# Optimization experiments

Hardware: AMD Instinct MI355X
Metric: run time of the kernel (lower is better)

## Reference

```python
import jax, jax.numpy as jnp
import numpy as np

B, NUMS, SEQ, H, LAYERS, PRED = 128, 128, 256, 1024, 2, 96


def setup_inputs() -> dict:
    key = jax.random.key(0)
    ks = jax.random.split(key, 7)
    s = 0.02
    return {
        "x": jax.random.normal(ks[0], (B, NUMS, SEQ), jnp.float32),
        "W0": jax.random.normal(ks[1], (NUMS + H, 4 * H), jnp.float32) * s,
        "b0": jax.random.normal(ks[2], (4 * H,), jnp.float32) * s,
        "W1": jax.random.normal(ks[3], (H + H, 4 * H), jnp.float32) * s,
        "b1": jax.random.normal(ks[4], (4 * H,), jnp.float32) * s,
        "fc_w": jax.random.normal(ks[5], (H, PRED), jnp.float32) * s,
        "fc_b": jax.random.normal(ks[6], (PRED,), jnp.float32) * s,
    }


def _lstm_layer(x_seq, W, b, h0, c0):
    # x_seq: [B, T, D]; W packs the four gate linears [D+H, 4H] (i,f,o,g)
    def step(carry, xt):
        h, c = carry
        z = jnp.concatenate([xt, h], axis=1) @ W + b  # [B, 4H]
        i, f, o, g = jnp.split(z, 4, axis=1)
        i, f, o = jax.nn.sigmoid(i), jax.nn.sigmoid(f), jax.nn.sigmoid(o)
        c = f * c + i * jnp.tanh(g)
        h = o * jnp.tanh(c)
        return (h, c), h

    (h, c), hs = jax.lax.scan(step, (h0, c0), jnp.swapaxes(x_seq, 0, 1))
    return jnp.swapaxes(hs, 0, 1), h, c  # [B, T, H], [B, H], [B, H]


def reference(x, W0, b0, W1, b1, fc_w, fc_b):
    bsz = x.shape[0]
    h = jnp.zeros((bsz, H), x.dtype)
    c = jnp.zeros((bsz, H), x.dtype)
    seq = jnp.swapaxes(x, 1, 2)  # [B, T, NUMS]
    # NB: faithful to source, (h, c) carry over across layers (no reset)
    seq, h, c = _lstm_layer(seq, W0, b0, h, c)
    seq, h, c = _lstm_layer(seq, W1, b1, h, c)
    out = jnp.tanh(seq[:, -1, :] @ fc_w + fc_b)  # [B, PRED]
    return (out, h, c)
```

## Files before the change

kernel.cpp:

```cpp
#include <hip/hip_runtime.h>
#include <stdint.h>

#define Bsz  128
#define NUMS 128
#define SEQn 256
#define Hn   1024
#define PRED 96
#define G4H  4096
#define GN   256
#define BH   ((size_t)Bsz*Hn)

typedef __attribute__((ext_vector_type(8))) short bf16x8;
typedef __attribute__((ext_vector_type(4))) float f32x4;

template<int N> struct IC { static constexpr int value = N; };

__device__ __forceinline__ unsigned short f2bf(float x){
  union { float f; unsigned u; } v; v.f = x;
  return (unsigned short)((v.u + 0x7FFFu + ((v.u >> 16) & 1u)) >> 16);
}
__device__ __forceinline__ float bf2f(unsigned short s){
  union { unsigned u; float f; } v; v.u = ((unsigned)s) << 16; return v.f;
}

__global__ void pack_x_kernel(const float* __restrict__ x, unsigned short* __restrict__ xp){
  __shared__ float tile[64][65];
  const int t0 = blockIdx.x * 64, n0 = blockIdx.y * 64, b = blockIdx.z;
  const int tid = threadIdx.x;
  const int c = tid & 63, r = tid >> 6;
  #pragma unroll
  for (int i = 0; i < 16; i++){
    int n = r + i*4;
    tile[n][c] = x[((size_t)b*NUMS + n0 + n)*SEQn + t0 + c];
  }
  __syncthreads();
  #pragma unroll
  for (int i = 0; i < 16; i++){
    int t = r + i*4;
    xp[((size_t)(t0+t)*Bsz + b)*NUMS + n0 + c] = f2bf(tile[c][t]);
  }
}

__global__ void pack_w_kernel(const float* __restrict__ W, unsigned short* __restrict__ Wpk,
                              int KST, int row_off, int kstride, int kof){
  const int u = blockIdx.x * blockDim.x + threadIdx.x;
  if (u >= 256*KST*64) return;
  const int lane = u & 63;
  const int kst  = (u >> 6) % KST;
  const int cgg  = (u >> 6) / KST;
  const int nb = cgg >> 2, gate = cgg & 3;
  const int col = gate*Hn + nb*16 + (lane & 15);
  const int kbase = row_off + kst*32 + (lane >> 4)*8;
  unsigned short tmp[8];
  #pragma unroll
  for (int e = 0; e < 8; e++) tmp[e] = f2bf(W[(size_t)(kbase+e)*G4H + col]);
  ((ulonglong2*)Wpk)[(size_t)(cgg*kstride + kof + kst)*64 + lane] = *(const ulonglong2*)tmp;
}

__global__ void zero_kernel(unsigned short* __restrict__ h0, float* __restrict__ c,
                            unsigned* __restrict__ bars){
  int i = blockIdx.x*256 + threadIdx.x;
  if (i < Bsz*Hn){ h0[i] = 0; c[i] = 0.0f; }
  if (i < 512) bars[i] = 0u;
}

template<int K1, int S2, int KTOT, int LAYER, bool RING2>
__global__ __launch_bounds__(512, 2)
void persist_kernel(const unsigned short* __restrict__ xpp,
                    unsigned short* __restrict__ hring,
                    unsigned short* __restrict__ h1b,
                    const unsigned short* __restrict__ Wpk,
                    const float* __restrict__ bias,
                    float* __restrict__ cst,
                    float* __restrict__ hf_out,
                    unsigned* __restrict__ bar)
{
  constexpr int KST_TOT = KTOT/32;
  constexpr int HALF = KST_TOT/2;
  constexpr int NCH = (KTOT + 511)/512;
  __shared__ union SM {
    struct { unsigned short a[2][32*512]; unsigned short xb[32*128]; } s;
    float e[2][4*32*18];
  } sm;
  const int tid = threadIdx.x;
  const int w = tid >> 6, l = tid & 63;
  const int blk = blockIdx.x;
  const int q = blk >> 3;
  const int nb = (blk & 7)*8 + (q & 7);
  const int mb = q >> 3;
  const int ksh = w & 1, cgi = w >> 1;
  const int cgg = nb*4 + cgi;
  const int lrow = l & 15, lg = l >> 4;

  bf16x8 wreg[HALF];
  #pragma unroll
  for (int j = 0; j < HALF; j++)
    wreg[j] = *(const bf16x8*)(Wpk + ((size_t)(cgg*KST_TOT + 2*j + ksh)*64 + l)*8);

  const int erow = tid >> 4, ejj = tid & 15;
  const int R = mb*32 + erow;
  const int J = nb*16 + ejj;
  const size_t idx = (size_t)R*Hn + J;
  float creg = (LAYER == 0) ? 0.f : cst[idx];

  for (int t = 0; t < SEQn; ++t){
    #pragma unroll
    for (int j = 0; j < HALF; j++) asm volatile("" : "+v"(wreg[j]));

    const unsigned short* A1;
    const unsigned short* A2;
    unsigned short* hout;
    if (LAYER == 0){
      A1   = hring + (size_t)t*BH;
      A2   = xpp + (size_t)t*Bsz*NUMS;
      hout = hring + (size_t)(t+1)*BH;
    } else {
      A1   = hring + (size_t)(t+1)*BH;
      A2   = (t == 0) ? (hring + (size_t)SEQn*BH)
                      : (h1b + (size_t)(RING2 ? (t-1) : ((t-1)&1))*BH);
      hout = h1b + (size_t)(RING2 ? t : (t&1))*BH;
    }

    f32x4 acc2[2] = {{0.f,0.f,0.f,0.f},{0.f,0.f,0.f,0.f}};

    auto stage = [&](int ch, int kw, int lu,
                     const unsigned short* A1p, const unsigned short* A2p){
      unsigned short* dst = (LAYER == 0 && ch == NCH-1) ? sm.s.xb : sm.s.a[ch & 1];
      const int nissue = kw >> 4;
      for (int i = w; i < nissue; i += 8){
        const int s = i*64 + l;
        const int row = s >> lu;
        const int uu  = s & ((1 << lu) - 1);
        const int ku  = uu ^ (row & 7);
        const int kg  = ch*512 + ku*8;
        const int Rr  = mb*32 + row;
        if (kg < K1){
          const unsigned short* src = A1p + (size_t)Rr*K1 + kg;
          __builtin_amdgcn_global_load_lds(
            (const __attribute__((address_space(1))) void*)src,
            (__attribute__((address_space(3))) void*)&dst[i*512], 16, 0, 0);
        } else {
          const unsigned short* src = A2p + (size_t)Rr*S2 + (kg - K1);
          if constexpr (LAYER == 1 && !RING2){
            __builtin_amdgcn_global_load_lds(
              (const __attribute__((address_space(1))) void*)src,
              (__attribute__((address_space(3))) void*)&dst[i*512], 16, 0, 17);
          } else {
            __builtin_amdgcn_global_load_lds(
              (const __attribute__((address_space(1))) void*)src,
              (__attribute__((address_space(3))) void*)&dst[i*512], 16, 0, 0);
          }
        }
      }
    };

    const bool pre01 = (LAYER == 1) && (t > 0);
    const bool preX  = (LAYER == 0) && (t > 0);
    if (!pre01){
      constexpr int kw0 = (KTOT >= 512) ? 512 : KTOT;
      stage(0, kw0, (kw0 == 512) ? 6 : 4, A1, A2);
    }
    __syncthreads();

    auto do_chunk = [&](auto CHC){
      constexpr int ch = decltype(CHC)::value;
      if constexpr (ch < NCH){
        constexpr int kw = ((KTOT - ch*512) >= 512) ? 512 : (KTOT - ch*512);
        if constexpr (ch + 1 < NCH){
          constexpr int kwn = ((KTOT - (ch+1)*512) >= 512) ? 512 : (KTOT - (ch+1)*512);
          const bool skip = (pre01 && (ch+1) == 1) || (preX && (ch+1) == NCH-1);
          if (!skip) stage(ch+1, kwn, (kwn == 512) ? 6 : 4, A1, A2);
        }
        constexpr int UPR  = kw >> 3;
        constexpr int nksl = kw >> 6;
        const unsigned short* abase = (LAYER == 0 && ch == NCH-1) ? sm.s.xb
                                                                  : sm.s.a[ch & 1];
        #pragma unroll
        for (int ksl = 0; ksl < nksl; ksl++){
          const int klocal = ksl*2 + ksh;
          const int unit = klocal*4 + lg;
          bf16x8 af0 = *(const bf16x8*)&abase[((lrow     )*UPR + (unit ^ (lrow & 7)))*8];
          bf16x8 af1 = *(const bf16x8*)&abase[((lrow + 16)*UPR + (unit ^ (lrow & 7)))*8];
          acc2[0] = __builtin_amdgcn_mfma_f32_16x16x32_bf16(af0, wreg[ch*8 + ksl], acc2[0], 0, 0, 0);
          acc2[1] = __builtin_amdgcn_mfma_f32_16x16x32_bf16(af1, wreg[ch*8 + ksl], acc2[1], 0, 0, 0);
        }
        __syncthreads();
      }
    };
    do_chunk(IC<0>{}); do_chunk(IC<1>{}); do_chunk(IC<2>{}); do_chunk(IC<3>{});

    {
      #pragma unroll
      for (int mi = 0; mi < 2; mi++)
        #pragma unroll
        for (int r = 0; r < 4; r++){
          const int row2 = mi*16 + lg*4 + r;
          sm.e[ksh][(cgi*32 + row2)*18 + lrow] = acc2[mi][r];
        }
    }
    __syncthreads();
    {
      float zi = sm.e[0][(0*32+erow)*18 + ejj] + sm.e[1][(0*32+erow)*18 + ejj];
      float zf = sm.e[0][(1*32+erow)*18 + ejj] + sm.e[1][(1*32+erow)*18 + ejj];
      float zo = sm.e[0][(2*32+erow)*18 + ejj] + sm.e[1][(2*32+erow)*18 + ejj];
      float zg = sm.e[0][(3*32+erow)*18 + ejj] + sm.e[1][(3*32+erow)*18 + ejj];
      zi += bias[0*Hn + J]; zf += bias[1*Hn + J];
      zo += bias[2*Hn + J]; zg += bias[3*Hn + J];
      const float gi = 1.f/(1.f + __expf(-zi));
      const float gf = 1.f/(1.f + __expf(-zf));
      const float go = 1.f/(1.f + __expf(-zo));
      const float gg = tanhf(zg);
      creg = gf * creg + gi * gg;
      const float hn = go * tanhf(creg);
      const unsigned hu   = (unsigned)f2bf(hn);
      const unsigned mate = (unsigned)__shfl_xor((int)hu, 1);
      if ((l & 1) == 0){
        const unsigned pk = hu | (mate << 16);
        __hip_atomic_store((unsigned*)(hout + idx), pk,
                           __ATOMIC_RELAXED, __HIP_MEMORY_SCOPE_AGENT);
      }
      if (t == SEQn-1){
        cst[idx] = creg;
        if (LAYER == 1) hf_out[idx] = hn;
      }
    }

    if (t + 1 < SEQn){
      __syncthreads();
      if (tid == 0)
        __hip_atomic_fetch_add(&bar[t], 1u, __ATOMIC_RELAXED, __HIP_MEMORY_SCOPE_AGENT);
      if constexpr (LAYER == 1){
        const unsigned short* A1n = hring + (size_t)(t+2)*BH;
        stage(0, 512, 6, A1n, A1n);
        stage(1, 512, 6, A1n, A1n);
      } else {
        stage(NCH-1, 128, 4, A1, xpp + (size_t)(t+1)*Bsz*NUMS);
      }
      if (tid == 0){
        while (__hip_atomic_load(&bar[t], __ATOMIC_RELAXED, __HIP_MEMORY_SCOPE_AGENT) < GN)
          __builtin_amdgcn_s_sleep(1);
      }
      __syncthreads();
    }
  }
}

__global__ __launch_bounds__(256)
void fc_out_kernel(const float* __restrict__ hf, const float* __restrict__ cst,
                   const float* __restrict__ fcw, const float* __restrict__ fcb,
                   float* __restrict__ dout){
  __shared__ float hrow[Hn];
  const int b = blockIdx.x, tid = threadIdx.x;
  for (int i = tid; i < Hn; i += 256) hrow[i] = hf[(size_t)b*Hn + i];
  __syncthreads();
  if (tid < PRED){
    float a = fcb[tid];
    for (int k = 0; k < Hn; k++) a += hrow[k] * fcw[(size_t)k*PRED + tid];
    dout[(size_t)b*PRED + tid] = tanhf(a);
  }
  for (int i = tid; i < Hn; i += 256){
    dout[Bsz*PRED + (size_t)b*Hn + i] = hf[(size_t)b*Hn + i];
    dout[Bsz*PRED + (size_t)Bsz*Hn + (size_t)b*Hn + i] = cst[(size_t)b*Hn + i];
  }
}

extern "C" void kernel_launch(void* const* d_in, const int* in_sizes, int n_in,
                              void* d_out, int out_size, void* d_ws, size_t ws_size,
                              hipStream_t stream){
  const float* x   = (const float*)d_in[0];
  const float* W0  = (const float*)d_in[1];
  const float* b0  = (const float*)d_in[2];
  const float* W1  = (const float*)d_in[3];
  const float* b1  = (const float*)d_in[4];
  const float* fcw = (const float*)d_in[5];
  const float* fcb = (const float*)d_in[6];
  float* dout = (float*)d_out;

  char* p = (char*)d_ws;
  auto alloc = [&](size_t bytes)->void*{
    void* r = (void*)p; p += (bytes + 255) & ~(size_t)255; return r;
  };
  unsigned short* xp   = (unsigned short*)alloc((size_t)SEQn*Bsz*NUMS*2);
  unsigned short* Wpk0 = (unsigned short*)alloc((size_t)256*36*64*8*2);
  unsigned short* Wpk1 = (unsigned short*)alloc((size_t)256*64*64*8*2);
  unsigned short* H0   = (unsigned short*)alloc((size_t)(SEQn+1)*BH*2);
  float* cst = (float*)alloc((size_t)BH*4);
  float* hf  = (float*)alloc((size_t)BH*4);
  unsigned* bars = (unsigned*)alloc((size_t)512*sizeof(unsigned));

  const bool big = ws_size >= (size_t)176*1024*1024;
  unsigned short* h1b;
  if (big) h1b = (unsigned short*)alloc((size_t)SEQn*BH*2);
  else     h1b = (unsigned short*)alloc((size_t)2*BH*2);

  pack_x_kernel<<<dim3(SEQn/64, NUMS/64, Bsz), dim3(256), 0, stream>>>(x, xp);
  pack_w_kernel<<<dim3((256*32*64 + 255)/256), dim3(256), 0, stream>>>(W0, Wpk0, 32, 128, 36, 0);
  pack_w_kernel<<<dim3((256*4*64  + 255)/256), dim3(256), 0, stream>>>(W0, Wpk0,  4,   0, 36, 32);
  pack_w_kernel<<<dim3((256*64*64 + 255)/256), dim3(256), 0, stream>>>(W1, Wpk1, 64, 0, 64, 0);
  zero_kernel<<<dim3((Bsz*Hn + 255)/256), dim3(256), 0, stream>>>(H0, cst, bars);

  persist_kernel<1024, NUMS, 1152, 0, false><<<dim3(GN), dim3(512), 0, stream>>>(
      xp, H0, nullptr, Wpk0, b0, cst, nullptr, bars);

  if (big){
    persist_kernel<1024, Hn, 2048, 1, true><<<dim3(GN), dim3(512), 0, stream>>>(
        nullptr, H0, h1b, Wpk1, b1, cst, hf, bars + 256);
  } else {
    persist_kernel<1024, Hn, 2048, 1, false><<<dim3(GN), dim3(512), 0, stream>>>(
        nullptr, H0, h1b, Wpk1, b1, cst, hf, bars + 256);
  }

  fc_out_kernel<<<dim3(Bsz), dim3(256), 0, stream>>>(hf, cst, fcw, fcb, dout);
}
```

Measured before the change: 3.528 ms.

## Split grid barrier per batch-row group and issue all chunk loads upfront with vmcnt waits

The global per-timestep barrier over all 256 blocks becomes four independent barriers, one per batch-row group (mb), since each group only depends on its own rows of h. Shared memory now holds every K chunk at once, so all async global-to-LDS loads are issued at the start of the step and consumed in order using explicit vmcnt waits, replacing the double-buffered chunk loop with its per-chunk __syncthreads. Bias loads are hoisted out of the time loop. The larger LDS footprint may hurt occupancy, and the hand-set vmcnt counts must match the issued load count exactly.

```diff
diff --git a/kernel.cpp b/kernel.cpp
--- a/kernel.cpp
+++ b/kernel.cpp
@@ -19,9 +19,11 @@
   union { float f; unsigned u; } v; v.f = x;
   return (unsigned short)((v.u + 0x7FFFu + ((v.u >> 16) & 1u)) >> 16);
 }
-__device__ __forceinline__ float bf2f(unsigned short s){
-  union { unsigned u; float f; } v; v.u = ((unsigned)s) << 16; return v.f;
-}
+
+#define WAITV(N) do { \
+  asm volatile("s_waitcnt vmcnt(" #N ")" ::: "memory"); \
+  __builtin_amdgcn_sched_barrier(0); \
+  __builtin_amdgcn_s_barrier(); } while(0)
 
 __global__ void pack_x_kernel(const float* __restrict__ x, unsigned short* __restrict__ xp){
   __shared__ float tile[64][65];
@@ -61,7 +63,7 @@
                             unsigned* __restrict__ bars){
   int i = blockIdx.x*256 + threadIdx.x;
   if (i < Bsz*Hn){ h0[i] = 0; c[i] = 0.0f; }
-  if (i < 512) bars[i] = 0u;
+  if (i < 2048) bars[i] = 0u;
 }
 
 template<int K1, int S2, int KTOT, int LAYER, bool RING2>
@@ -77,11 +79,11 @@
 {
   constexpr int KST_TOT = KTOT/32;
   constexpr int HALF = KST_TOT/2;
-  constexpr int NCH = (KTOT + 511)/512;
-  __shared__ union SM {
-    struct { unsigned short a[2][32*512]; unsigned short xb[32*128]; } s;
-    float e[2][4*32*18];
-  } sm;
+  constexpr int NFULL = (LAYER == 0) ? 2 : 4;
+  __shared__ unsigned short sa[NFULL][32*512];
+  __shared__ unsigned short sxb[(LAYER == 0) ? 32*128 : 64];
+  __shared__ float se[2][4*32*18];
+
   const int tid = threadIdx.x;
   const int w = tid >> 6, l = tid & 63;
   const int blk = blockIdx.x;
@@ -102,6 +104,48 @@
   const int J = nb*16 + ejj;
   const size_t idx = (size_t)R*Hn + J;
   float creg = (LAYER == 0) ? 0.f : cst[idx];
+  const float bI = bias[0*Hn + J], bF = bias[1*Hn + J];
+  const float bO = bias[2*Hn + J], bG = bias[3*Hn + J];
+
+  auto stageFull = [&](int ch, const unsigned short* A1p, const unsigned short* A2p){
+    unsigned short* dst = sa[ch];
+    #pragma unroll
+    for (int ii = 0; ii < 4; ii++){
+      const int i = ii*8 + w;
+      const int s = i*64 + l;
+      const int row = s >> 6, uu = s & 63;
+      const int ku  = uu ^ (row & 7);
+      const int kg  = ch*512 + ku*8;
+      const int Rr  = mb*32 + row;
+      if (kg < K1){
+        const unsigned short* src = A1p + (size_t)Rr*K1 + kg;
+        __builtin_amdgcn_global_load_lds(
+          (const __attribute__((address_space(1))) void*)src,
+          (__attribute__((address_space(3))) void*)&dst[i*512], 16, 0, 0);
+      } else {
+        const unsigned short* src = A2p + (size_t)Rr*S2 + (kg - K1);
+        if constexpr (LAYER == 1 && !RING2){
+          __builtin_amdgcn_global_load_lds(
+            (const __attribute__((address_space(1))) void*)src,
+            (__attribute__((address_space(3))) void*)&dst[i*512], 16, 0, 17);
+        } else {
+          __builtin_amdgcn_global_load_lds(
+            (const __attribute__((address_space(1))) void*)src,
+            (__attribute__((address_space(3))) void*)&dst[i*512], 16, 0, 0);
+        }
+      }
+    }
+  };
+  auto stageXB = [&](const unsigned short* A2p){
+    const int i = w;
+    const int s = i*64 + l;
+    const int row = s >> 4, uu = s & 15;
+    const int ku  = uu ^ (row & 7);
+    const unsigned short* src = A2p + (size_t)(mb*32 + row)*S2 + ku*8;
+    __builtin_amdgcn_global_load_lds(
+      (const __attribute__((address_space(1))) void*)src,
+      (__attribute__((address_space(3))) void*)&sxb[i*512], 16, 0, 0);
+  };
 
   for (int t = 0; t < SEQn; ++t){
     #pragma unroll
@@ -123,71 +167,46 @@
 
     f32x4 acc2[2] = {{0.f,0.f,0.f,0.f},{0.f,0.f,0.f,0.f}};
 
-    auto stage = [&](int ch, int kw, int lu,
-                     const unsigned short* A1p, const unsigned short* A2p){
-      unsigned short* dst = (LAYER == 0 && ch == NCH-1) ? sm.s.xb : sm.s.a[ch & 1];
-      const int nissue = kw >> 4;
-      for (int i = w; i < nissue; i += 8){
-        const int s = i*64 + l;
-        const int row = s >> lu;
-        const int uu  = s & ((1 << lu) - 1);
-        const int ku  = uu ^ (row & 7);
-        const int kg  = ch*512 + ku*8;
-        const int Rr  = mb*32 + row;
-        if (kg < K1){
-          const unsigned short* src = A1p + (size_t)Rr*K1 + kg;
-          __builtin_amdgcn_global_load_lds(
-            (const __attribute__((address_space(1))) void*)src,
-            (__attribute__((address_space(3))) void*)&dst[i*512], 16, 0, 0);
-        } else {
-          const unsigned short* src = A2p + (size_t)Rr*S2 + (kg - K1);
-          if constexpr (LAYER == 1 && !RING2){
-            __builtin_amdgcn_global_load_lds(
-              (const __attribute__((address_space(1))) void*)src,
-              (__attribute__((address_space(3))) void*)&dst[i*512], 16, 0, 17);
-          } else {
-            __builtin_amdgcn_global_load_lds(
-              (const __attribute__((address_space(1))) void*)src,
-              (__attribute__((address_space(3))) void*)&dst[i*512], 16, 0, 0);
-          }
-        }
+    if constexpr (LAYER == 1){
+      if (t == 0){ stageFull(0, A1, A2); stageFull(1, A1, A2); }
+      stageFull(2, A1, A2); stageFull(3, A1, A2);
+    } else {
+      if (t == 0) stageXB(A2);
+      stageFull(0, A1, A2); stageFull(1, A1, A2);
+    }
+
+    auto comp = [&](auto CHC){
+      constexpr int ch = decltype(CHC)::value;
+      const unsigned short* abase = sa[ch];
+      #pragma unroll
+      for (int ksl = 0; ksl < 8; ksl++){
+        const int klocal = ksl*2 + ksh;
+        const int unit = klocal*4 + lg;
+        bf16x8 af0 = *(const bf16x8*)&abase[((lrow     )*64 + (unit ^ (lrow & 7)))*8];
+        bf16x8 af1 = *(const bf16x8*)&abase[((lrow + 16)*64 + (unit ^ (lrow & 7)))*8];
+        acc2[0] = __builtin_amdgcn_mfma_f32_16x16x32_bf16(af0, wreg[ch*8 + ksl], acc2[0], 0, 0, 0);
+        acc2[1] = __builtin_amdgcn_mfma_f32_16x16x32_bf16(af1, wreg[ch*8 + ksl], acc2[1], 0, 0, 0);
       }
     };
 
-    const bool pre01 = (LAYER == 1) && (t > 0);
-    const bool preX  = (LAYER == 0) && (t > 0);
-    if (!pre01){
-      constexpr int kw0 = (KTOT >= 512) ? 512 : KTOT;
-      stage(0, kw0, (kw0 == 512) ? 6 : 4, A1, A2);
-    }
-    __syncthreads();
-
-    auto do_chunk = [&](auto CHC){
-      constexpr int ch = decltype(CHC)::value;
-      if constexpr (ch < NCH){
-        constexpr int kw = ((KTOT - ch*512) >= 512) ? 512 : (KTOT - ch*512);
-        if constexpr (ch + 1 < NCH){
-          constexpr int kwn = ((KTOT - (ch+1)*512) >= 512) ? 512 : (KTOT - (ch+1)*512);
-          const bool skip = (pre01 && (ch+1) == 1) || (preX && (ch+1) == NCH-1);
-          if (!skip) stage(ch+1, kwn, (kwn == 512) ? 6 : 4, A1, A2);
-        }
-        constexpr int UPR  = kw >> 3;
-        constexpr int nksl = kw >> 6;
-        const unsigned short* abase = (LAYER == 0 && ch == NCH-1) ? sm.s.xb
-                                                                  : sm.s.a[ch & 1];
-        #pragma unroll
-        for (int ksl = 0; ksl < nksl; ksl++){
-          const int klocal = ksl*2 + ksh;
-          const int unit = klocal*4 + lg;
-          bf16x8 af0 = *(const bf16x8*)&abase[((lrow     )*UPR + (unit ^ (lrow & 7)))*8];
-          bf16x8 af1 = *(const bf16x8*)&abase[((lrow + 16)*UPR + (unit ^ (lrow & 7)))*8];
-          acc2[0] = __builtin_amdgcn_mfma_f32_16x16x32_bf16(af0, wreg[ch*8 + ksl], acc2[0], 0, 0, 0);
-          acc2[1] = __builtin_amdgcn_mfma_f32_16x16x32_bf16(af1, wreg[ch*8 + ksl], acc2[1], 0, 0, 0);
-        }
-        __syncthreads();
-      }
-    };
-    do_chunk(IC<0>{}); do_chunk(IC<1>{}); do_chunk(IC<2>{}); do_chunk(IC<3>{});
+    if constexpr (LAYER == 1){
+      WAITV(12); comp(IC<0>{});
+      WAITV(8);  comp(IC<1>{});
+      WAITV(4);  comp(IC<2>{});
+      WAITV(0);  comp(IC<3>{});
+    } else {
+      WAITV(4);  comp(IC<0>{});
+      WAITV(0);  comp(IC<1>{});
+      #pragma unroll
+      for (int ksl = 0; ksl < 2; ksl++){
+        const int klocal = ksl*2 + ksh;
+        const int unit = klocal*4 + lg;
+        bf16x8 af0 = *(const bf16x8*)&sxb[((lrow     )*16 + (unit ^ (lrow & 7)))*8];
+        bf16x8 af1 = *(const bf16x8*)&sxb[((lrow + 16)*16 + (unit ^ (lrow & 7)))*8];
+        acc2[0] = __builtin_amdgcn_mfma_f32_16x16x32_bf16(af0, wreg[16 + ksl], acc2[0], 0, 0, 0);
+        acc2[1] = __builtin_amdgcn_mfma_f32_16x16x32_bf16(af1, wreg[16 + ksl], acc2[1], 0, 0, 0);
+      }
+    }
 
     {
       #pragma unroll
@@ -195,17 +214,15 @@
         #pragma unroll
         for (int r = 0; r < 4; r++){
           const int row2 = mi*16 + lg*4 + r;
-          sm.e[ksh][(cgi*32 + row2)*18 + lrow] = acc2[mi][r];
+          se[ksh][(cgi*32 + row2)*18 + lrow] = acc2[mi][r];
         }
     }
     __syncthreads();
     {
-      float zi = sm.e[0][(0*32+erow)*18 + ejj] + sm.e[1][(0*32+erow)*18 + ejj];
-      float zf = sm.e[0][(1*32+erow)*18 + ejj] + sm.e[1][(1*32+erow)*18 + ejj];
-      float zo = sm.e[0][(2*32+erow)*18 + ejj] + sm.e[1][(2*32+erow)*18 + ejj];
-      float zg = sm.e[0][(3*32+erow)*18 + ejj] + sm.e[1][(3*32+erow)*18 + ejj];
-      zi += bias[0*Hn + J]; zf += bias[1*Hn + J];
-      zo += bias[2*Hn + J]; zg += bias[3*Hn + J];
+      float zi = se[0][(0*32+erow)*18 + ejj] + se[1][(0*32+erow)*18 + ejj] + bI;
+      float zf = se[0][(1*32+erow)*18 + ejj] + se[1][(1*32+erow)*18 + ejj] + bF;
+      float zo = se[0][(2*32+erow)*18 + ejj] + se[1][(2*32+erow)*18 + ejj] + bO;
+      float zg = se[0][(3*32+erow)*18 + ejj] + se[1][(3*32+erow)*18 + ejj] + bG;
       const float gi = 1.f/(1.f + __expf(-zi));
       const float gf = 1.f/(1.f + __expf(-zf));
       const float go = 1.f/(1.f + __expf(-zo));
@@ -228,19 +245,21 @@
     if (t + 1 < SEQn){
       __syncthreads();
       if (tid == 0)
-        __hip_atomic_fetch_add(&bar[t], 1u, __ATOMIC_RELAXED, __HIP_MEMORY_SCOPE_AGENT);
+        __hip_atomic_fetch_add(&bar[t*4 + mb], 1u,
+                               __ATOMIC_RELAXED, __HIP_MEMORY_SCOPE_AGENT);
       if constexpr (LAYER == 1){
         const unsigned short* A1n = hring + (size_t)(t+2)*BH;
-        stage(0, 512, 6, A1n, A1n);
-        stage(1, 512, 6, A1n, A1n);
+        stageFull(0, A1n, A1n);
+        stageFull(1, A1n, A1n);
       } else {
-        stage(NCH-1, 128, 4, A1, xpp + (size_t)(t+1)*Bsz*NUMS);
+        stageXB(xpp + (size_t)(t+1)*Bsz*NUMS);
       }
       if (tid == 0){
-        while (__hip_atomic_load(&bar[t], __ATOMIC_RELAXED, __HIP_MEMORY_SCOPE_AGENT) < GN)
+        while (__hip_atomic_load(&bar[t*4 + mb], __ATOMIC_RELAXED,
+                                 __HIP_MEMORY_SCOPE_AGENT) < 64u)
           __builtin_amdgcn_s_sleep(1);
       }
-      __syncthreads();
+      __builtin_amdgcn_s_barrier();
     }
   }
 }
@@ -286,7 +305,7 @@
   unsigned short* H0   = (unsigned short*)alloc((size_t)(SEQn+1)*BH*2);
   float* cst = (float*)alloc((size_t)BH*4);
   float* hf  = (float*)alloc((size_t)BH*4);
-  unsigned* bars = (unsigned*)alloc((size_t)512*sizeof(unsigned));
+  unsigned* bars = (unsigned*)alloc((size_t)2048*sizeof(unsigned));
 
   const bool big = ws_size >= (size_t)176*1024*1024;
   unsigned short* h1b;
@@ -304,10 +323,10 @@
 
   if (big){
     persist_kernel<1024, Hn, 2048, 1, true><<<dim3(GN), dim3(512), 0, stream>>>(
-        nullptr, H0, h1b, Wpk1, b1, cst, hf, bars + 256);
+        nullptr, H0, h1b, Wpk1, b1, cst, hf, bars + 1024);
   } else {
     persist_kernel<1024, Hn, 2048, 1, false><<<dim3(GN), dim3(512), 0, stream>>>(
-        nullptr, H0, h1b, Wpk1, b1, cst, hf, bars + 256);
+        nullptr, H0, h1b, Wpk1, b1, cst, hf, bars + 1024);
   }
 
   fc_out_kernel<<<dim3(Bsz), dim3(256), 0, stream>>>(hf, cst, fcw, fcb, dout);
```

New measurement: 4.657 ms. 32.0% more time.

## Stage all K chunks in separate LDS buffers and drop per-chunk barriers

Applied to the files above, without the earlier changes.

Each K chunk now gets its own shared-memory buffer instead of ping-ponging two buffers. All chunks are issued up front, which removes the per-chunk __syncthreads. On later timesteps, work that depends on already-available data (the x input in layer 0, the layer-0 h in layer 1) is computed first while the recurrent-h chunks are loaded, leaving a single barrier before the remaining MFMAs. Layer 1 quadruples its A staging buffers, which raises LDS use and may limit the two-blocks-per-CU occupancy, and the barrier array is enlarged.

```diff
diff --git a/kernel.cpp b/kernel.cpp
--- a/kernel.cpp
+++ b/kernel.cpp
@@ -18,9 +18,6 @@
 __device__ __forceinline__ unsigned short f2bf(float x){
   union { float f; unsigned u; } v; v.f = x;
   return (unsigned short)((v.u + 0x7FFFu + ((v.u >> 16) & 1u)) >> 16);
-}
-__device__ __forceinline__ float bf2f(unsigned short s){
-  union { unsigned u; float f; } v; v.u = ((unsigned)s) << 16; return v.f;
 }
 
 __global__ void pack_x_kernel(const float* __restrict__ x, unsigned short* __restrict__ xp){
@@ -61,7 +58,7 @@
                             unsigned* __restrict__ bars){
   int i = blockIdx.x*256 + threadIdx.x;
   if (i < Bsz*Hn){ h0[i] = 0; c[i] = 0.0f; }
-  if (i < 512) bars[i] = 0u;
+  if (i < 1024) bars[i] = 0u;
 }
 
 template<int K1, int S2, int KTOT, int LAYER, bool RING2>
@@ -78,10 +75,11 @@
   constexpr int KST_TOT = KTOT/32;
   constexpr int HALF = KST_TOT/2;
   constexpr int NCH = (KTOT + 511)/512;
-  __shared__ union SM {
-    struct { unsigned short a[2][32*512]; unsigned short xb[32*128]; } s;
-    float e[2][4*32*18];
-  } sm;
+  constexpr int NBUF = (LAYER == 0) ? 2 : 4;
+  __shared__ unsigned short sa[NBUF][32*512];
+  __shared__ unsigned short sxb[(LAYER == 0) ? 32*128 : 64];
+  __shared__ float se[2][4*32*18];
+
   const int tid = threadIdx.x;
   const int w = tid >> 6, l = tid & 63;
   const int blk = blockIdx.x;
@@ -125,7 +123,7 @@
 
     auto stage = [&](int ch, int kw, int lu,
                      const unsigned short* A1p, const unsigned short* A2p){
-      unsigned short* dst = (LAYER == 0 && ch == NCH-1) ? sm.s.xb : sm.s.a[ch & 1];
+      unsigned short* dst = (LAYER == 0 && ch == NCH-1) ? sxb : sa[ch];
       const int nissue = kw >> 4;
       for (int i = w; i < nissue; i += 8){
         const int s = i*64 + l;
@@ -154,27 +152,14 @@
       }
     };
 
-    const bool pre01 = (LAYER == 1) && (t > 0);
-    const bool preX  = (LAYER == 0) && (t > 0);
-    if (!pre01){
-      constexpr int kw0 = (KTOT >= 512) ? 512 : KTOT;
-      stage(0, kw0, (kw0 == 512) ? 6 : 4, A1, A2);
-    }
-    __syncthreads();
-
-    auto do_chunk = [&](auto CHC){
+    auto comp = [&](auto CHC){
       constexpr int ch = decltype(CHC)::value;
       if constexpr (ch < NCH){
-        constexpr int kw = ((KTOT - ch*512) >= 512) ? 512 : (KTOT - ch*512);
-        if constexpr (ch + 1 < NCH){
-          constexpr int kwn = ((KTOT - (ch+1)*512) >= 512) ? 512 : (KTOT - (ch+1)*512);
-          const bool skip = (pre01 && (ch+1) == 1) || (preX && (ch+1) == NCH-1);
-          if (!skip) stage(ch+1, kwn, (kwn == 512) ? 6 : 4, A1, A2);
-        }
+        constexpr bool isx = (LAYER == 0 && ch == NCH-1);
+        constexpr int kw   = isx ? 128 : 512;
         constexpr int UPR  = kw >> 3;
         constexpr int nksl = kw >> 6;
-        const unsigned short* abase = (LAYER == 0 && ch == NCH-1) ? sm.s.xb
-                                                                  : sm.s.a[ch & 1];
+        const unsigned short* abase = isx ? sxb : sa[ch];
         #pragma unroll
         for (int ksl = 0; ksl < nksl; ksl++){
           const int klocal = ksl*2 + ksh;
@@ -184,10 +169,26 @@
           acc2[0] = __builtin_amdgcn_mfma_f32_16x16x32_bf16(af0, wreg[ch*8 + ksl], acc2[0], 0, 0, 0);
           acc2[1] = __builtin_amdgcn_mfma_f32_16x16x32_bf16(af1, wreg[ch*8 + ksl], acc2[1], 0, 0, 0);
         }
-        __syncthreads();
       }
     };
-    do_chunk(IC<0>{}); do_chunk(IC<1>{}); do_chunk(IC<2>{}); do_chunk(IC<3>{});
+
+    if (t == 0){
+      stage(0, 512, 6, A1, A2); stage(1, 512, 6, A1, A2);
+      if constexpr (LAYER == 1){ stage(2, 512, 6, A1, A2); stage(3, 512, 6, A1, A2); }
+      else                       stage(2, 128, 4, A1, A2);
+      __syncthreads();
+      comp(IC<0>{}); comp(IC<1>{}); comp(IC<2>{}); comp(IC<3>{});
+    } else if constexpr (LAYER == 1){
+      stage(2, 512, 6, A1, A2); stage(3, 512, 6, A1, A2);
+      comp(IC<0>{}); comp(IC<1>{});
+      __syncthreads();
+      comp(IC<2>{}); comp(IC<3>{});
+    } else {
+      stage(0, 512, 6, A1, A2); stage(1, 512, 6, A1, A2);
+      comp(IC<2>{});
+      __syncthreads();
+      comp(IC<0>{}); comp(IC<1>{});
+    }
 
     {
       #pragma unroll
@@ -195,15 +196,15 @@
         #pragma unroll
         for (int r = 0; r < 4; r++){
           const int row2 = mi*16 + lg*4 + r;
-          sm.e[ksh][(cgi*32 + row2)*18 + lrow] = acc2[mi][r];
+          se[ksh][(cgi*32 + row2)*18 + lrow] = acc2[mi][r];
         }
     }
     __syncthreads();
     {
-      float zi = sm.e[0][(0*32+erow)*18 + ejj] + sm.e[1][(0*32+erow)*18 + ejj];
-      float zf = sm.e[0][(1*32+erow)*18 + ejj] + sm.e[1][(1*32+erow)*18 + ejj];
-      float zo = sm.e[0][(2*32+erow)*18 + ejj] + sm.e[1][(2*32+erow)*18 + ejj];
-      float zg = sm.e[0][(3*32+erow)*18 + ejj] + sm.e[1][(3*32+erow)*18 + ejj];
+      float zi = se[0][(0*32+erow)*18 + ejj] + se[1][(0*32+erow)*18 + ejj];
+      float zf = se[0][(1*32+erow)*18 + ejj] + se[1][(1*32+erow)*18 + ejj];
+      float zo = se[0][(2*32+erow)*18 + ejj] + se[1][(2*32+erow)*18 + ejj];
+      float zg = se[0][(3*32+erow)*18 + ejj] + se[1][(3*32+erow)*18 + ejj];
       zi += bias[0*Hn + J]; zf += bias[1*Hn + J];
       zo += bias[2*Hn + J]; zg += bias[3*Hn + J];
       const float gi = 1.f/(1.f + __expf(-zi));
@@ -286,7 +287,7 @@
   unsigned short* H0   = (unsigned short*)alloc((size_t)(SEQn+1)*BH*2);
   float* cst = (float*)alloc((size_t)BH*4);
   float* hf  = (float*)alloc((size_t)BH*4);
-  unsigned* bars = (unsigned*)alloc((size_t)512*sizeof(unsigned));
+  unsigned* bars = (unsigned*)alloc((size_t)1024*sizeof(unsigned));
 
   const bool big = ws_size >= (size_t)176*1024*1024;
   unsigned short* h1b;
@@ -304,10 +305,10 @@
 
   if (big){
     persist_kernel<1024, Hn, 2048, 1, true><<<dim3(GN), dim3(512), 0, stream>>>(
-        nullptr, H0, h1b, Wpk1, b1, cst, hf, bars + 256);
+        nullptr, H0, h1b, Wpk1, b1, cst, hf, bars + 512);
   } else {
     persist_kernel<1024, Hn, 2048, 1, false><<<dim3(GN), dim3(512), 0, stream>>>(
-        nullptr, H0, h1b, Wpk1, b1, cst, hf, bars + 256);
+        nullptr, H0, h1b, Wpk1, b1, cst, hf, bars + 512);
   }
 
   fc_out_kernel<<<dim3(Bsz), dim3(256), 0, stream>>>(hf, cst, fcw, fcb, dout);
```

Result: no change. 3.595 ms (+1.9%).
